# Optimization experiments

Hardware: AMD Instinct MI355X
Metric: run time of the kernel (lower is better)

## Reference

```python
import jax, jax.numpy as jnp
import numpy as np

N_SRC = 100000

def setup_inputs() -> dict:
    key = jax.random.key(0)
    k1, k2, k3 = jax.random.split(key, 3)
    feat_src = jax.random.normal(k1, (N_SRC, 64), dtype=jnp.float32)
    edge_src = jax.random.randint(k2, (1250000,), 0, N_SRC, dtype=jnp.int64)
    edge_dst = jax.random.randint(k3, (1250000,), 0, 50000, dtype=jnp.int64)
    return {"feat_src": feat_src, "edge_src": edge_src, "edge_dst": edge_dst, "n_dst": 50000}

def reference(feat_src, edge_src, edge_dst, n_dst):
    n_src = feat_src.shape[0]
    ones = jnp.ones(edge_src.shape[0], dtype=feat_src.dtype)
    # out-degree of src nodes, in-degree of dst nodes
    deg_out = jax.ops.segment_sum(ones, edge_src, num_segments=n_src)
    deg_in = jax.ops.segment_sum(ones, edge_dst, num_segments=n_dst)
    norm_src = jax.lax.rsqrt(jnp.clip(deg_out, 1.0))  # [n_src]
    norm_dst = jax.lax.rsqrt(jnp.clip(deg_in, 1.0))   # [n_dst]
    # gather -> scale -> scatter-sum
    msg = feat_src[edge_src] * norm_src[edge_src][:, None]      # [E, d]
    rst = jax.ops.segment_sum(msg, edge_dst, num_segments=n_dst)  # [n_dst, d]
    return rst * norm_dst[:, None]
```

## Files before the change

kernel.cpp:

```cpp
#include <hip/hip_runtime.h>

#define NFEAT 64
#define SCAN_BLOCKS 128

#define PRANGE 25600
#define PWORDS (PRANGE / 2)
#define NB_IN  128
#define NB_OUT 64

__global__ __launch_bounds__(1024) void v27_hist(
        const int* __restrict__ idx, unsigned short* __restrict__ cnt,
        int E, int n, int Ec) {
    __shared__ int lh[PWORDS];
    int b = blockIdx.x, t = threadIdx.x, T = blockDim.x;
    int rbase = blockIdx.y * PRANGE;
    int rend = rbase + PRANGE; if (rend > n) rend = n;
    int W = rend - rbase;
    if (W <= 0) return;
    int Wp = (W + 1) >> 1;
    for (int i = t; i < Wp; i += T) lh[i] = 0;
    __syncthreads();
    int lo = b * Ec;
    int hi = lo + Ec; if (hi > E) hi = E;
    if (lo < hi) {
        int cntE = hi - lo;
        int nq = cntE >> 2;
#define V27_H(val)                                                            \
        {                                                                     \
            unsigned r = (unsigned)((val) - rbase);                           \
            if (r < (unsigned)W)                                              \
                atomicAdd(&lh[r >> 1], 1 << ((r & 1) << 4));                  \
        }
        for (int q = t; q < nq; q += T) {
            int i = lo + (q << 2);
            int4 e = *(const int4*)(idx + i);
            V27_H(e.x) V27_H(e.y) V27_H(e.z) V27_H(e.w)
        }
        for (int i = lo + (nq << 2) + t; i < hi; i += T) V27_H(idx[i]);
#undef V27_H
    }
    __syncthreads();
    unsigned short* row = cnt + (size_t)b * n + rbase;
    if ((((size_t)b * n + rbase) & 1) == 0) {
        unsigned* row32 = (unsigned*)row;
        int full = W >> 1;
        for (int i = t; i < full; i += T) row32[i] = (unsigned)lh[i];
        if ((W & 1) && t == 0)
            row[W - 1] = (unsigned short)(lh[W >> 1] & 0xffff);
    } else {
        for (int i = t; i < W; i += T)
            row[i] = (unsigned short)((lh[i >> 1] >> ((i & 1) << 4)) & 0xffff);
    }
}

__global__ void v27_norm(const unsigned short* __restrict__ cnt_out,
                         unsigned short* __restrict__ cnt_in,
                         int* __restrict__ deg_in,
                         float* __restrict__ nsrc, float* __restrict__ ndst,
                         int n_src, int n_dst) {
    int i = blockIdx.x * blockDim.x + threadIdx.x;
    if (i < n_src) {
        const unsigned short* p = cnt_out + i;
        int s = 0;
        for (int b = 0; b < NB_OUT; ++b) { s += *p; p += n_src; }
        nsrc[i] = rsqrtf(fmaxf((float)s, 1.0f));
    }
    if (i < n_dst) {
        unsigned short* p = cnt_in + i;
        int a = 0;
        for (int b = 0; b < NB_IN; ++b) {
            int c = *p;
            *p = (unsigned short)a;
            a += c;
            p += n_dst;
        }
        deg_in[i] = a;
        ndst[i] = rsqrtf(fmaxf((float)a, 1.0f));
    }
}

__global__ __launch_bounds__(1024) void v27_place(
        const int* __restrict__ esrc, const int* __restrict__ edst,
        const unsigned short* __restrict__ pre, const int* __restrict__ row_start,
        int* __restrict__ sorted_src, int E, int n_dst, int Ec) {
    __shared__ int lh[PWORDS];
    int b = blockIdx.x, t = threadIdx.x, T = blockDim.x;
    int rbase = blockIdx.y * PRANGE;
    int rend = rbase + PRANGE; if (rend > n_dst) rend = n_dst;
    int W = rend - rbase;
    if (W <= 0) return;
    int Wp = (W + 1) >> 1;
    for (int i = t; i < Wp; i += T) lh[i] = 0;
    __syncthreads();
    int lo = b * Ec;
    int hi = lo + Ec; if (hi > E) hi = E;
    if (lo >= hi) return;
    const unsigned short* prow = pre + (size_t)b * n_dst;
    int cntE = hi - lo;
    int nq = cntE >> 2;
#define V27_PL(dd, ss)                                                        \
    {                                                                         \
        unsigned r = (unsigned)((dd) - rbase);                                \
        if (r < (unsigned)W) {                                                \
            int sh = (r & 1) << 4;                                            \
            int old = atomicAdd(&lh[r >> 1], 1 << sh);                        \
            int rank = (old >> sh) & 0xffff;                                  \
            int slot = row_start[dd] + (int)prow[dd] + rank;                  \
            if ((unsigned)slot < (unsigned)E) sorted_src[slot] = (ss);        \
        }                                                                     \
    }
    for (int q = t; q < nq; q += T) {
        int i = lo + (q << 2);
        int4 dv = *(const int4*)(edst + i);
        int4 sv = *(const int4*)(esrc + i);
        V27_PL(dv.x, sv.x)
        V27_PL(dv.y, sv.y)
        V27_PL(dv.z, sv.z)
        V27_PL(dv.w, sv.w)
    }
    for (int i = lo + (nq << 2) + t; i < hi; i += T) {
        int d = edst[i];
        int s = esrc[i];
        V27_PL(d, s)
    }
#undef V27_PL
}

__global__ void v26_gather(const float* __restrict__ feat,
                           const int* __restrict__ sorted_src,
                           const int* __restrict__ row_start,
                           const float* __restrict__ nsrc,
                           const float* __restrict__ ndst,
                           float* __restrict__ out,
                           int n_src, int n_dst) {
    int gid = blockIdx.x * blockDim.x + threadIdx.x;
    int d = gid >> 6;
    if (d >= n_dst) return;
    int lane = threadIdx.x & 63;
    int g = lane >> 4;
    int lg = lane & 15;
    int lo = row_start[d], hi = row_start[d + 1];
    int nmax = n_src - 1;
    float4 a0 = {0,0,0,0}, a1 = {0,0,0,0}, a2 = {0,0,0,0}, a3 = {0,0,0,0};
#define V26_G(kk, acc)                                                        \
    {                                                                         \
        int s_ = sorted_src[(kk) + g];                                        \
        s_ = min(max(s_, 0), nmax);                                           \
        float w_ = nsrc[s_];                                                  \
        float4 v_ = *(const float4*)(feat + (size_t)s_ * NFEAT + (lg << 2));  \
        acc.x += v_.x * w_; acc.y += v_.y * w_;                               \
        acc.z += v_.z * w_; acc.w += v_.w * w_;                               \
    }
    int k = lo;
    for (; k + 15 < hi; k += 16) {
        V26_G(k, a0)
        V26_G(k + 4, a1)
        V26_G(k + 8, a2)
        V26_G(k + 12, a3)
    }
    for (; k + 3 < hi; k += 4) {
        V26_G(k, a0)
    }
    if (k + g < hi) {
        V26_G(k, a1)
    }
#undef V26_G
    float4 a;
    a.x = (a0.x + a1.x) + (a2.x + a3.x);
    a.y = (a0.y + a1.y) + (a2.y + a3.y);
    a.z = (a0.z + a1.z) + (a2.z + a3.z);
    a.w = (a0.w + a1.w) + (a2.w + a3.w);
    a.x += __shfl_xor(a.x, 16); a.x += __shfl_xor(a.x, 32);
    a.y += __shfl_xor(a.y, 16); a.y += __shfl_xor(a.y, 32);
    a.z += __shfl_xor(a.z, 16); a.z += __shfl_xor(a.z, 32);
    a.w += __shfl_xor(a.w, 16); a.w += __shfl_xor(a.w, 32);
    if (g == 0) {
        float sc = ndst[d];
        float4 r;
        r.x = a.x * sc; r.y = a.y * sc; r.z = a.z * sc; r.w = a.w * sc;
        *(float4*)(out + (size_t)d * NFEAT + (lg << 2)) = r;
    }
}


__global__ void v23_scan1(const int* __restrict__ deg_in, int* __restrict__ bsum,
                          int n_dst, int chunk) {
    __shared__ int red[256];
    int b = blockIdx.x, t = threadIdx.x;
    int lo = b * chunk;
    int hi = lo + chunk; if (hi > n_dst) hi = n_dst;
    int s = 0;
    for (int i = lo + t; i < hi; i += 256) s += deg_in[i];
    red[t] = s;
    __syncthreads();
    for (int o = 128; o > 0; o >>= 1) {
        if (t < o) red[t] += red[t + o];
        __syncthreads();
    }
    if (t == 0) bsum[b] = red[0];
}

__global__ void v23_scan2(int* __restrict__ bsum, int* __restrict__ boff,
                          int* __restrict__ row_start, int n_dst) {
    if (threadIdx.x == 0) {
        int a = 0;
        for (int k = 0; k < SCAN_BLOCKS; ++k) { boff[k] = a; a += bsum[k]; }
        row_start[n_dst] = a;
    }
}

__global__ void v23_scan3(const int* __restrict__ deg_in, const int* __restrict__ boff,
                          int* __restrict__ row_start, int* __restrict__ cursor,
                          int n_dst, int chunk) {
    __shared__ int tsum[256];
    int b = blockIdx.x, t = threadIdx.x;
    int lo = b * chunk;
    int hi = lo + chunk; if (hi > n_dst) hi = n_dst;
    int per = (chunk + 255) / 256;
    int mylo = lo + t * per;
    int myhi = mylo + per; if (myhi > hi) myhi = hi;
    int s = 0;
    for (int i = mylo; i < myhi; ++i) s += deg_in[i];
    tsum[t] = s;
    __syncthreads();
    if (t == 0) {
        int a = 0;
        for (int k = 0; k < 256; ++k) { int v = tsum[k]; tsum[k] = a; a += v; }
    }
    __syncthreads();
    int a = boff[b] + tsum[t];
    for (int i = mylo; i < myhi; ++i) {
        row_start[i] = a;
        cursor[i] = a;
        a += deg_in[i];
    }
}


__global__ void v23_zero(int* __restrict__ deg_out, int* __restrict__ deg_in,
                         int n_src, int n_dst) {
    int i = blockIdx.x * blockDim.x + threadIdx.x;
    if (i < n_src) deg_out[i] = 0;
    if (i < n_dst) deg_in[i] = 0;
}

__global__ void v23_deg(const int* __restrict__ esrc, const int* __restrict__ edst,
                        int* __restrict__ deg_out, int* __restrict__ deg_in,
                        int E, int n_src, int n_dst) {
    int i = blockIdx.x * blockDim.x + threadIdx.x;
    if (i >= E) return;
    int s = esrc[i];
    int d = edst[i];
    if ((unsigned)s < (unsigned)n_src) atomicAdd(&deg_out[s], 1);
    if ((unsigned)d < (unsigned)n_dst) atomicAdd(&deg_in[d], 1);
}

__global__ void v23_norm(const int* __restrict__ deg_out, const int* __restrict__ deg_in,
                         float* __restrict__ nsrc, float* __restrict__ ndst,
                         int n_src, int n_dst) {
    int i = blockIdx.x * blockDim.x + threadIdx.x;
    if (i < n_src) nsrc[i] = rsqrtf(fmaxf((float)deg_out[i], 1.0f));
    if (i < n_dst) ndst[i] = rsqrtf(fmaxf((float)deg_in[i], 1.0f));
}

__global__ void v23_place(const int* __restrict__ esrc, const int* __restrict__ edst,
                          int* __restrict__ cursor, int* __restrict__ sorted_src,
                          int E, int n_src, int n_dst) {
    int i = blockIdx.x * blockDim.x + threadIdx.x;
    if (i >= E) return;
    int s = esrc[i];
    int d = edst[i];
    if ((unsigned)s >= (unsigned)n_src) return;
    if ((unsigned)d >= (unsigned)n_dst) return;
    int slot = atomicAdd(&cursor[d], 1);
    sorted_src[slot] = s;
}


extern "C" void kernel_launch(void* const* d_in, const int* in_sizes, int n_in,
                              void* d_out, int out_size, void* d_ws, size_t ws_size,
                              hipStream_t stream) {
    const float* feat = (const float*)d_in[0];
    const int* esrc = (const int*)d_in[1];
    const int* edst = (const int*)d_in[2];
    float* out = (float*)d_out;

    const int n_src = in_sizes[0] / NFEAT;
    const int E     = in_sizes[1];
    const int n_dst = out_size / NFEAT;

    const int B = 256;
    int nmax = n_src > n_dst ? n_src : n_dst;
    int chunk = (n_dst + SCAN_BLOCKS - 1) / SCAN_BLOCKS;

    size_t sz_cnt_in  = ((size_t)NB_IN  * (size_t)n_dst * 2 + 255) & ~(size_t)255;
    size_t sz_cnt_out = ((size_t)NB_OUT * (size_t)n_src * 2 + 255) & ~(size_t)255;
    size_t sz_fixed = (size_t)E * 4
                    + (size_t)n_dst * 4
                    + (size_t)n_src * 4
                    + (size_t)n_dst * 4
                    + (size_t)n_dst * 4
                    + (size_t)(n_dst + 1) * 4
                    + (size_t)SCAN_BLOCKS * 8 + 512;
    bool big = ws_size >= sz_cnt_in + sz_cnt_out + sz_fixed;

    if (big) {
        char* ws = (char*)d_ws;
        size_t off = 0;
        unsigned short* cnt_in  = (unsigned short*)(ws + off); off += sz_cnt_in;
        unsigned short* cnt_out = (unsigned short*)(ws + off); off += sz_cnt_out;
        int*   sorted_src = (int*)(ws + off);   off += (size_t)E * 4;
        int*   deg_in     = (int*)(ws + off);   off += (size_t)n_dst * 4;
        float* nsrc       = (float*)(ws + off); off += (size_t)n_src * 4;
        float* ndst       = (float*)(ws + off); off += (size_t)n_dst * 4;
        int*   cursor     = (int*)(ws + off);   off += (size_t)n_dst * 4;
        int*   row_start  = (int*)(ws + off);   off += (size_t)(n_dst + 1) * 4;
        int*   bsum       = (int*)(ws + off);   off += SCAN_BLOCKS * 4;
        int*   boff       = (int*)(ws + off);   off += SCAN_BLOCKS * 4;

        int Ec_in  = (((E + NB_IN  - 1) / NB_IN ) + 3) & ~3;
        int Ec_out = (((E + NB_OUT - 1) / NB_OUT) + 3) & ~3;
        int P_in  = (n_dst + PRANGE - 1) / PRANGE;
        int P_out = (n_src + PRANGE - 1) / PRANGE;

        dim3 gout(NB_OUT, P_out), gin(NB_IN, P_in);

        v27_hist<<<gout, 1024, 0, stream>>>(esrc, cnt_out, E, n_src, Ec_out);
        v27_hist<<<gin,  1024, 0, stream>>>(edst, cnt_in,  E, n_dst, Ec_in);
        v27_norm<<<(nmax + B - 1) / B, B, 0, stream>>>(cnt_out, cnt_in, deg_in,
                                                       nsrc, ndst, n_src, n_dst);
        v23_scan1<<<SCAN_BLOCKS, B, 0, stream>>>(deg_in, bsum, n_dst, chunk);
        v23_scan2<<<1, 64, 0, stream>>>(bsum, boff, row_start, n_dst);
        v23_scan3<<<SCAN_BLOCKS, B, 0, stream>>>(deg_in, boff, row_start, cursor,
                                                 n_dst, chunk);
        v27_place<<<gin, 1024, 0, stream>>>(esrc, edst, cnt_in, row_start,
                                            sorted_src, E, n_dst, Ec_in);
        long long gthreads = (long long)n_dst * 64;
        v26_gather<<<(int)((gthreads + B - 1) / B), B, 0, stream>>>(feat, sorted_src,
                                                                    row_start, nsrc, ndst,
                                                                    out, n_src, n_dst);
    } else {
        char* ws = (char*)d_ws;
        size_t off = 0;
        int*   deg_out    = (int*)(ws + off);   off += (size_t)n_src * 4;
        int*   deg_in     = (int*)(ws + off);   off += (size_t)n_dst * 4;
        float* nsrc       = (float*)(ws + off); off += (size_t)n_src * 4;
        float* ndst       = (float*)(ws + off); off += (size_t)n_dst * 4;
        int*   row_start  = (int*)(ws + off);   off += (size_t)(n_dst + 1) * 4;
        int*   cursor     = (int*)(ws + off);   off += (size_t)n_dst * 4;
        int*   bsum       = (int*)(ws + off);   off += SCAN_BLOCKS * 4;
        int*   boff       = (int*)(ws + off);   off += SCAN_BLOCKS * 4;
        int*   sorted_src = (int*)(ws + off);   off += (size_t)E * 4;

        v23_zero<<<(nmax + B - 1) / B, B, 0, stream>>>(deg_out, deg_in, n_src, n_dst);
        v23_deg<<<(E + B - 1) / B, B, 0, stream>>>(esrc, edst, deg_out, deg_in,
                                                   E, n_src, n_dst);
        v23_norm<<<(nmax + B - 1) / B, B, 0, stream>>>(deg_out, deg_in, nsrc, ndst,
                                                       n_src, n_dst);
        v23_scan1<<<SCAN_BLOCKS, B, 0, stream>>>(deg_in, bsum, n_dst, chunk);
        v23_scan2<<<1, 64, 0, stream>>>(bsum, boff, row_start, n_dst);
        v23_scan3<<<SCAN_BLOCKS, B, 0, stream>>>(deg_in, boff, row_start, cursor,
                                                 n_dst, chunk);
        v23_place<<<(E + B - 1) / B, B, 0, stream>>>(esrc, edst, cursor, sorted_src,
                                                     E, n_src, n_dst);
        long long gthreads = (long long)n_dst * 64;
        v26_gather<<<(int)((gthreads + B - 1) / B), B, 0, stream>>>(feat, sorted_src,
                                                                    row_start, nsrc, ndst,
                                                                    out, n_src, n_dst);
    }
}
```

Baseline: 188.8 us.

## Use byte-wide per-chunk degree counters and fuse histogram, norm and scan kernels

Per-chunk degree histograms shrink from 16-bit to 8-bit counters packed four per LDS word, roughly halving the count arrays that are written and then re-read. The two histogram launches become one grid. The norm pass now also produces the block sums, and a new row-start kernel computes its own block offset, which removes the separate scan kernels. The place kernel covers the full destination range in one LDS pass. The trade-off is that any per-chunk count or any destination's in-degree of 256 or more will silently wrap, and the big path now requires node counts that fit the fixed LDS size.

```diff
diff --git a/kernel.cpp b/kernel.cpp
--- a/kernel.cpp
+++ b/kernel.cpp
@@ -3,127 +3,170 @@
 #define NFEAT 64
 #define SCAN_BLOCKS 128
 
-#define PRANGE 25600
-#define PWORDS (PRANGE / 2)
 #define NB_IN  128
 #define NB_OUT 64
-
-__global__ __launch_bounds__(1024) void v27_hist(
-        const int* __restrict__ idx, unsigned short* __restrict__ cnt,
-        int E, int n, int Ec) {
-    __shared__ int lh[PWORDS];
-    int b = blockIdx.x, t = threadIdx.x, T = blockDim.x;
-    int rbase = blockIdx.y * PRANGE;
-    int rend = rbase + PRANGE; if (rend > n) rend = n;
-    int W = rend - rbase;
+#define LWORDS 12512
+
+__global__ __launch_bounds__(1024) void v28_hist(
+        const int* __restrict__ esrc, const int* __restrict__ edst,
+        unsigned char* __restrict__ cnt_in, unsigned char* __restrict__ cnt_out,
+        int E, int n_src, int n_dst, int Ec_in, int Ec_out, int srange) {
+    __shared__ unsigned int lh[LWORDS];
+    int blk = blockIdx.x, t = threadIdx.x, T = blockDim.x;
+    const int* idx; unsigned char* row; int rbase, W, lo, hi;
+    if (blk < NB_IN) {
+        idx = edst; rbase = 0; W = n_dst;
+        row = cnt_in + (size_t)blk * n_dst;
+        lo = blk * Ec_in; hi = lo + Ec_in;
+    } else {
+        int p    = (blk - NB_IN) / NB_OUT;
+        int brel = (blk - NB_IN) % NB_OUT;
+        idx = esrc; rbase = p * srange;
+        W = n_src - rbase; if (W > srange) W = srange;
+        row = cnt_out + (size_t)brel * n_src + rbase;
+        lo = brel * Ec_out; hi = lo + Ec_out;
+    }
+    if (hi > E) hi = E;
     if (W <= 0) return;
-    int Wp = (W + 1) >> 1;
+    int Wp = (W + 3) >> 2;
     for (int i = t; i < Wp; i += T) lh[i] = 0;
     __syncthreads();
-    int lo = b * Ec;
-    int hi = lo + Ec; if (hi > E) hi = E;
     if (lo < hi) {
-        int cntE = hi - lo;
-        int nq = cntE >> 2;
-#define V27_H(val)                                                            \
+        int nq = (hi - lo) >> 2;
+#define V28_H(val)                                                            \
         {                                                                     \
             unsigned r = (unsigned)((val) - rbase);                           \
             if (r < (unsigned)W)                                              \
-                atomicAdd(&lh[r >> 1], 1 << ((r & 1) << 4));                  \
+                atomicAdd(&lh[r >> 2], 1u << ((r & 3) << 3));                 \
         }
         for (int q = t; q < nq; q += T) {
             int i = lo + (q << 2);
             int4 e = *(const int4*)(idx + i);
-            V27_H(e.x) V27_H(e.y) V27_H(e.z) V27_H(e.w)
+            V28_H(e.x) V28_H(e.y) V28_H(e.z) V28_H(e.w)
         }
-        for (int i = lo + (nq << 2) + t; i < hi; i += T) V27_H(idx[i]);
-#undef V27_H
-    }
-    __syncthreads();
-    unsigned short* row = cnt + (size_t)b * n + rbase;
-    if ((((size_t)b * n + rbase) & 1) == 0) {
-        unsigned* row32 = (unsigned*)row;
-        int full = W >> 1;
-        for (int i = t; i < full; i += T) row32[i] = (unsigned)lh[i];
-        if ((W & 1) && t == 0)
-            row[W - 1] = (unsigned short)(lh[W >> 1] & 0xffff);
+        for (int i = lo + (nq << 2) + t; i < hi; i += T) V28_H(idx[i]);
+#undef V28_H
+    }
+    __syncthreads();
+    if ((((uintptr_t)row) & 3) == 0 && (W & 3) == 0) {
+        unsigned int* row32 = (unsigned int*)row;
+        for (int i = t; i < Wp; i += T) row32[i] = lh[i];
     } else {
         for (int i = t; i < W; i += T)
-            row[i] = (unsigned short)((lh[i >> 1] >> ((i & 1) << 4)) & 0xffff);
-    }
-}
-
-__global__ void v27_norm(const unsigned short* __restrict__ cnt_out,
-                         unsigned short* __restrict__ cnt_in,
-                         int* __restrict__ deg_in,
-                         float* __restrict__ nsrc, float* __restrict__ ndst,
-                         int n_src, int n_dst) {
-    int i = blockIdx.x * blockDim.x + threadIdx.x;
-    if (i < n_src) {
-        const unsigned short* p = cnt_out + i;
+            row[i] = (unsigned char)((lh[i >> 2] >> ((i & 3) << 3)) & 0xff);
+    }
+}
+
+__global__ void v28_normscan(const unsigned char* __restrict__ cnt_out,
+                             unsigned char* __restrict__ cnt_in,
+                             int* __restrict__ deg_in,
+                             float* __restrict__ nsrc, float* __restrict__ ndst,
+                             int* __restrict__ bsum, int n_src, int n_dst) {
+    __shared__ int red[256];
+    int b = blockIdx.x, t = threadIdx.x;
+    int cs = (n_src + SCAN_BLOCKS - 1) / SCAN_BLOCKS;
+    int slo = b * cs, shi = slo + cs; if (shi > n_src) shi = n_src;
+    for (int i = slo + t; i < shi; i += 256) {
+        const unsigned char* p = cnt_out + i;
         int s = 0;
-        for (int b = 0; b < NB_OUT; ++b) { s += *p; p += n_src; }
+        for (int j = 0; j < NB_OUT; ++j) { s += *p; p += n_src; }
         nsrc[i] = rsqrtf(fmaxf((float)s, 1.0f));
     }
-    if (i < n_dst) {
-        unsigned short* p = cnt_in + i;
+    int cd = (n_dst + SCAN_BLOCKS - 1) / SCAN_BLOCKS;
+    int dlo = b * cd, dhi = dlo + cd; if (dhi > n_dst) dhi = n_dst;
+    int tot = 0;
+    for (int i = dlo + t; i < dhi; i += 256) {
+        unsigned char* p = cnt_in + i;
         int a = 0;
-        for (int b = 0; b < NB_IN; ++b) {
+        for (int j = 0; j < NB_IN; ++j) {
             int c = *p;
-            *p = (unsigned short)a;
+            *p = (unsigned char)a;
             a += c;
             p += n_dst;
         }
         deg_in[i] = a;
         ndst[i] = rsqrtf(fmaxf((float)a, 1.0f));
-    }
-}
-
-__global__ __launch_bounds__(1024) void v27_place(
+        tot += a;
+    }
+    red[t] = tot;
+    __syncthreads();
+    for (int o = 128; o > 0; o >>= 1) {
+        if (t < o) red[t] += red[t + o];
+        __syncthreads();
+    }
+    if (t == 0) bsum[b] = red[0];
+}
+
+__global__ void v28_rowstart(const int* __restrict__ deg_in,
+                             const int* __restrict__ bsum,
+                             int* __restrict__ row_start, int n_dst) {
+    __shared__ int tsum[256];
+    __shared__ int boffs;
+    int b = blockIdx.x, t = threadIdx.x;
+    int cd = (n_dst + SCAN_BLOCKS - 1) / SCAN_BLOCKS;
+    int lo = b * cd, hi = lo + cd; if (hi > n_dst) hi = n_dst;
+    if (t == 0) {
+        int a = 0;
+        for (int k = 0; k < b; ++k) a += bsum[k];
+        boffs = a;
+    }
+    int per = (cd + 255) / 256;
+    int mylo = lo + t * per;
+    int myhi = mylo + per; if (myhi > hi) myhi = hi;
+    int s = 0;
+    for (int i = mylo; i < myhi; ++i) s += deg_in[i];
+    tsum[t] = s;
+    __syncthreads();
+    if (t == 0) {
+        int a = 0;
+        for (int k = 0; k < 256; ++k) { int v = tsum[k]; tsum[k] = a; a += v; }
+    }
+    __syncthreads();
+    int a = boffs + tsum[t];
+    for (int i = mylo; i < myhi; ++i) { row_start[i] = a; a += deg_in[i]; }
+    if (b == SCAN_BLOCKS - 1 && t == 255) row_start[n_dst] = a;
+}
+
+__global__ __launch_bounds__(1024) void v28_place(
         const int* __restrict__ esrc, const int* __restrict__ edst,
-        const unsigned short* __restrict__ pre, const int* __restrict__ row_start,
+        const unsigned char* __restrict__ pre, const int* __restrict__ row_start,
         int* __restrict__ sorted_src, int E, int n_dst, int Ec) {
-    __shared__ int lh[PWORDS];
+    __shared__ unsigned int lh[LWORDS];
     int b = blockIdx.x, t = threadIdx.x, T = blockDim.x;
-    int rbase = blockIdx.y * PRANGE;
-    int rend = rbase + PRANGE; if (rend > n_dst) rend = n_dst;
-    int W = rend - rbase;
-    if (W <= 0) return;
-    int Wp = (W + 1) >> 1;
+    int Wp = (n_dst + 3) >> 2;
     for (int i = t; i < Wp; i += T) lh[i] = 0;
     __syncthreads();
     int lo = b * Ec;
     int hi = lo + Ec; if (hi > E) hi = E;
     if (lo >= hi) return;
-    const unsigned short* prow = pre + (size_t)b * n_dst;
-    int cntE = hi - lo;
-    int nq = cntE >> 2;
-#define V27_PL(dd, ss)                                                        \
-    {                                                                         \
-        unsigned r = (unsigned)((dd) - rbase);                                \
-        if (r < (unsigned)W) {                                                \
-            int sh = (r & 1) << 4;                                            \
-            int old = atomicAdd(&lh[r >> 1], 1 << sh);                        \
-            int rank = (old >> sh) & 0xffff;                                  \
-            int slot = row_start[dd] + (int)prow[dd] + rank;                  \
-            if ((unsigned)slot < (unsigned)E) sorted_src[slot] = (ss);        \
-        }                                                                     \
+    const unsigned char* prow = pre + (size_t)b * n_dst;
+    int nq = (hi - lo) >> 2;
+#define V28_PL(dd, ss)                                                       \
+    {                                                                        \
+        unsigned r = (unsigned)(dd);                                         \
+        if (r < (unsigned)n_dst) {                                           \
+            int sh = (r & 3) << 3;                                           \
+            unsigned old = atomicAdd(&lh[r >> 2], 1u << sh);                 \
+            int rank = (old >> sh) & 0xff;                                   \
+            int slot = row_start[r] + (int)prow[r] + rank;                   \
+            if ((unsigned)slot < (unsigned)E) sorted_src[slot] = (ss);       \
+        }                                                                    \
     }
     for (int q = t; q < nq; q += T) {
         int i = lo + (q << 2);
         int4 dv = *(const int4*)(edst + i);
         int4 sv = *(const int4*)(esrc + i);
-        V27_PL(dv.x, sv.x)
-        V27_PL(dv.y, sv.y)
-        V27_PL(dv.z, sv.z)
-        V27_PL(dv.w, sv.w)
+        V28_PL(dv.x, sv.x)
+        V28_PL(dv.y, sv.y)
+        V28_PL(dv.z, sv.z)
+        V28_PL(dv.w, sv.w)
     }
     for (int i = lo + (nq << 2) + t; i < hi; i += T) {
         int d = edst[i];
         int s = esrc[i];
-        V27_PL(d, s)
-    }
-#undef V27_PL
+        V28_PL(d, s)
+    }
+#undef V28_PL
 }
 
 __global__ void v26_gather(const float* __restrict__ feat,
@@ -183,6 +226,32 @@
 }
 
 
+__global__ void v23_zero(int* __restrict__ deg_out, int* __restrict__ deg_in,
+                         int n_src, int n_dst) {
+    int i = blockIdx.x * blockDim.x + threadIdx.x;
+    if (i < n_src) deg_out[i] = 0;
+    if (i < n_dst) deg_in[i] = 0;
+}
+
+__global__ void v23_deg(const int* __restrict__ esrc, const int* __restrict__ edst,
+                        int* __restrict__ deg_out, int* __restrict__ deg_in,
+                        int E, int n_src, int n_dst) {
+    int i = blockIdx.x * blockDim.x + threadIdx.x;
+    if (i >= E) return;
+    int s = esrc[i];
+    int d = edst[i];
+    if ((unsigned)s < (unsigned)n_src) atomicAdd(&deg_out[s], 1);
+    if ((unsigned)d < (unsigned)n_dst) atomicAdd(&deg_in[d], 1);
+}
+
+__global__ void v23_norm(const int* __restrict__ deg_out, const int* __restrict__ deg_in,
+                         float* __restrict__ nsrc, float* __restrict__ ndst,
+                         int n_src, int n_dst) {
+    int i = blockIdx.x * blockDim.x + threadIdx.x;
+    if (i < n_src) nsrc[i] = rsqrtf(fmaxf((float)deg_out[i], 1.0f));
+    if (i < n_dst) ndst[i] = rsqrtf(fmaxf((float)deg_in[i], 1.0f));
+}
+
 __global__ void v23_scan1(const int* __restrict__ deg_in, int* __restrict__ bsum,
                           int n_dst, int chunk) {
     __shared__ int red[256];
@@ -236,33 +305,6 @@
     }
 }
 
-
-__global__ void v23_zero(int* __restrict__ deg_out, int* __restrict__ deg_in,
-                         int n_src, int n_dst) {
-    int i = blockIdx.x * blockDim.x + threadIdx.x;
-    if (i < n_src) deg_out[i] = 0;
-    if (i < n_dst) deg_in[i] = 0;
-}
-
-__global__ void v23_deg(const int* __restrict__ esrc, const int* __restrict__ edst,
-                        int* __restrict__ deg_out, int* __restrict__ deg_in,
-                        int E, int n_src, int n_dst) {
-    int i = blockIdx.x * blockDim.x + threadIdx.x;
-    if (i >= E) return;
-    int s = esrc[i];
-    int d = edst[i];
-    if ((unsigned)s < (unsigned)n_src) atomicAdd(&deg_out[s], 1);
-    if ((unsigned)d < (unsigned)n_dst) atomicAdd(&deg_in[d], 1);
-}
-
-__global__ void v23_norm(const int* __restrict__ deg_out, const int* __restrict__ deg_in,
-                         float* __restrict__ nsrc, float* __restrict__ ndst,
-                         int n_src, int n_dst) {
-    int i = blockIdx.x * blockDim.x + threadIdx.x;
-    if (i < n_src) nsrc[i] = rsqrtf(fmaxf((float)deg_out[i], 1.0f));
-    if (i < n_dst) ndst[i] = rsqrtf(fmaxf((float)deg_in[i], 1.0f));
-}
-
 __global__ void v23_place(const int* __restrict__ esrc, const int* __restrict__ edst,
                           int* __restrict__ cursor, int* __restrict__ sorted_src,
                           int E, int n_src, int n_dst) {
@@ -293,48 +335,42 @@
     int nmax = n_src > n_dst ? n_src : n_dst;
     int chunk = (n_dst + SCAN_BLOCKS - 1) / SCAN_BLOCKS;
 
-    size_t sz_cnt_in  = ((size_t)NB_IN  * (size_t)n_dst * 2 + 255) & ~(size_t)255;
-    size_t sz_cnt_out = ((size_t)NB_OUT * (size_t)n_src * 2 + 255) & ~(size_t)255;
+    int srange = (((n_src + 1) / 2) + 3) & ~3;
+
+    size_t sz_cnt_in  = ((size_t)NB_IN  * (size_t)n_dst + 255) & ~(size_t)255;
+    size_t sz_cnt_out = ((size_t)NB_OUT * (size_t)n_src + 255) & ~(size_t)255;
     size_t sz_fixed = (size_t)E * 4
                     + (size_t)n_dst * 4
                     + (size_t)n_src * 4
                     + (size_t)n_dst * 4
+                    + (size_t)(n_dst + 1) * 4
                     + (size_t)n_dst * 4
-                    + (size_t)(n_dst + 1) * 4
                     + (size_t)SCAN_BLOCKS * 8 + 512;
-    bool big = ws_size >= sz_cnt_in + sz_cnt_out + sz_fixed;
+    bool big = (ws_size >= sz_cnt_in + sz_cnt_out + sz_fixed)
+             && (n_dst <= LWORDS * 4) && (srange <= LWORDS * 4);
 
     if (big) {
         char* ws = (char*)d_ws;
         size_t off = 0;
-        unsigned short* cnt_in  = (unsigned short*)(ws + off); off += sz_cnt_in;
-        unsigned short* cnt_out = (unsigned short*)(ws + off); off += sz_cnt_out;
+        unsigned char* cnt_in  = (unsigned char*)(ws + off); off += sz_cnt_in;
+        unsigned char* cnt_out = (unsigned char*)(ws + off); off += sz_cnt_out;
         int*   sorted_src = (int*)(ws + off);   off += (size_t)E * 4;
         int*   deg_in     = (int*)(ws + off);   off += (size_t)n_dst * 4;
         float* nsrc       = (float*)(ws + off); off += (size_t)n_src * 4;
         float* ndst       = (float*)(ws + off); off += (size_t)n_dst * 4;
-        int*   cursor     = (int*)(ws + off);   off += (size_t)n_dst * 4;
         int*   row_start  = (int*)(ws + off);   off += (size_t)(n_dst + 1) * 4;
         int*   bsum       = (int*)(ws + off);   off += SCAN_BLOCKS * 4;
-        int*   boff       = (int*)(ws + off);   off += SCAN_BLOCKS * 4;
 
         int Ec_in  = (((E + NB_IN  - 1) / NB_IN ) + 3) & ~3;
         int Ec_out = (((E + NB_OUT - 1) / NB_OUT) + 3) & ~3;
-        int P_in  = (n_dst + PRANGE - 1) / PRANGE;
-        int P_out = (n_src + PRANGE - 1) / PRANGE;
-
-        dim3 gout(NB_OUT, P_out), gin(NB_IN, P_in);
-
-        v27_hist<<<gout, 1024, 0, stream>>>(esrc, cnt_out, E, n_src, Ec_out);
-        v27_hist<<<gin,  1024, 0, stream>>>(edst, cnt_in,  E, n_dst, Ec_in);
-        v27_norm<<<(nmax + B - 1) / B, B, 0, stream>>>(cnt_out, cnt_in, deg_in,
-                                                       nsrc, ndst, n_src, n_dst);
-        v23_scan1<<<SCAN_BLOCKS, B, 0, stream>>>(deg_in, bsum, n_dst, chunk);
-        v23_scan2<<<1, 64, 0, stream>>>(bsum, boff, row_start, n_dst);
-        v23_scan3<<<SCAN_BLOCKS, B, 0, stream>>>(deg_in, boff, row_start, cursor,
-                                                 n_dst, chunk);
-        v27_place<<<gin, 1024, 0, stream>>>(esrc, edst, cnt_in, row_start,
-                                            sorted_src, E, n_dst, Ec_in);
+
+        v28_hist<<<NB_IN + 2 * NB_OUT, 1024, 0, stream>>>(
+            esrc, edst, cnt_in, cnt_out, E, n_src, n_dst, Ec_in, Ec_out, srange);
+        v28_normscan<<<SCAN_BLOCKS, B, 0, stream>>>(
+            cnt_out, cnt_in, deg_in, nsrc, ndst, bsum, n_src, n_dst);
+        v28_rowstart<<<SCAN_BLOCKS, B, 0, stream>>>(deg_in, bsum, row_start, n_dst);
+        v28_place<<<NB_IN, 1024, 0, stream>>>(esrc, edst, cnt_in, row_start,
+                                              sorted_src, E, n_dst, Ec_in);
         long long gthreads = (long long)n_dst * 64;
         v26_gather<<<(int)((gthreads + B - 1) / B), B, 0, stream>>>(feat, sorted_src,
                                                                     row_start, nsrc, ndst,
```

Result: slower. 205.4 us (+8.8%).
